# Optimization experiments

Hardware: AMD Instinct MI355X
Metric: run time of the kernel (lower is better)

Reference implementation:

```python
import jax, jax.numpy as jnp
import numpy as np

KH, KW = 2, 2  # kernel_shape: stride-2 zero-insertion unpool

def setup_inputs() -> dict:
    key = jax.random.key(0)
    x = jax.random.normal(key, (32, 112, 112, 64), dtype=jnp.float32)
    return {"x": x}

def reference(x) -> jnp.ndarray:
    # Equivalent to conv2d_transpose with identity-in-top-left kernel and
    # stride (KH, KW): each input element goes to the top-left of a KHxKW
    # zero block. Output shape: [B, H*KH, W*KW, C].
    b, h, w, c = x.shape
    out = jnp.zeros((b, h * KH, w * KW, c), dtype=x.dtype)
    out = out.at[:, ::KH, ::KW, :].set(x)
    return out
```

## Files before the change

### kernel.cpp

```cpp
#include <hip/hip_runtime.h>

typedef float f4 __attribute__((ext_vector_type(4)));

__global__ __launch_bounds__(256) void unpool_scatter(
    const f4* __restrict__ x, f4* __restrict__ out) {
    const int j = blockIdx.x * 256 + threadIdx.x;
    const int h = blockIdx.y;
    const int b = blockIdx.z;

    const f4* xrow = x + (size_t)(b * 112 + h) * 1792;
    f4* orow = out + (size_t)(b * 224 + 2 * h) * 3584;

    const f4 v = xrow[j];
    const int o = ((j & ~15) << 1) | (j & 15);
    __builtin_nontemporal_store(v, &orow[o]);
}

extern "C" void kernel_launch(void* const* d_in, const int* in_sizes, int n_in,
                              void* d_out, int out_size, void* d_ws, size_t ws_size,
                              hipStream_t stream) {
    hipMemsetAsync(d_out, 0, (size_t)out_size, stream);

    dim3 grid(7, 112, 32);
    dim3 block(256);
    unpool_scatter<<<grid, block, 0, stream>>>((const f4*)d_in[0], (f4*)d_out);
}
```

Measured before the change: 422.8 us.

## Fuse zero-fill into unpool kernel, writing full output rows directly

Removes the separate full-output memset and has each block write both the even output row (data interleaved with zeros) and the odd all-zero row. This avoids writing the data positions twice and saves a launch. The stores are no longer nontemporal, and each block holds 14 loaded vectors in registers.

```diff
diff --git a/kernel.cpp b/kernel.cpp
--- a/kernel.cpp
+++ b/kernel.cpp
@@ -2,26 +2,43 @@
 
 typedef float f4 __attribute__((ext_vector_type(4)));
 
-__global__ __launch_bounds__(256) void unpool_scatter(
+__global__ __launch_bounds__(256) void unpool_full(
     const f4* __restrict__ x, f4* __restrict__ out) {
-    const int j = blockIdx.x * 256 + threadIdx.x;
-    const int h = blockIdx.y;
-    const int b = blockIdx.z;
+    const int tid = threadIdx.x;
+    const int h   = blockIdx.x;
+    const int b   = blockIdx.y;
 
-    const f4* xrow = x + (size_t)(b * 112 + h) * 1792;
-    f4* orow = out + (size_t)(b * 224 + 2 * h) * 3584;
+    const f4* __restrict__ xrow = x + (size_t)(b * 112 + h) * 1792;
+    f4* __restrict__ orow_e = out + (size_t)(b * 224 + 2 * h) * 3584;
+    f4* __restrict__ orow_o = orow_e + 3584;
 
-    const f4 v = xrow[j];
-    const int o = ((j & ~15) << 1) | (j & 15);
-    __builtin_nontemporal_store(v, &orow[o]);
+    const int lane16  = tid & 15;
+    const int grp     = tid >> 5;
+    const bool is_data = ((tid >> 4) & 1) == 0;
+
+    f4 v[14];
+#pragma unroll
+    for (int k = 0; k < 14; ++k) {
+        v[k] = xrow[(grp + 8 * k) * 16 + lane16];
+    }
+
+    const f4 z = (f4){0.f, 0.f, 0.f, 0.f};
+
+#pragma unroll
+    for (int k = 0; k < 14; ++k) {
+        orow_o[tid + 256 * k] = z;
+    }
+
+#pragma unroll
+    for (int k = 0; k < 14; ++k) {
+        orow_e[tid + 256 * k] = is_data ? v[k] : z;
+    }
 }
 
 extern "C" void kernel_launch(void* const* d_in, const int* in_sizes, int n_in,
                               void* d_out, int out_size, void* d_ws, size_t ws_size,
                               hipStream_t stream) {
-    hipMemsetAsync(d_out, 0, (size_t)out_size, stream);
-
-    dim3 grid(7, 112, 32);
+    dim3 grid(112, 32);
     dim3 block(256);
-    unpool_scatter<<<grid, block, 0, stream>>>((const f4*)d_in[0], (f4*)d_out);
+    unpool_full<<<grid, block, 0, stream>>>((const f4*)d_in[0], (f4*)d_out);
 }
```

Measured after the change: 470.1 us. 11.2% more time.
